# Kernel tuning notes

Hardware: AMD Instinct MI355X
Metric: run time of the kernel (lower is better)

## Reference

```python
import jax, jax.numpy as jnp
import numpy as np

B, T, DIM = 1, 4096, 768
H, D = 6, 128  # num_heads, head_dim
ATTN_SCALE = 0.12
EPS = 1.1920929e-07  # torch fp32 rms_norm default eps


def _rms_norm(x):
    # F.rms_norm over last dim, no learned weight
    return x * jax.lax.rsqrt(jnp.mean(jnp.square(x), axis=-1, keepdims=True) + EPS)


def _rotary_tables(seq_len, head_dim):
    # angular_freq: (1/1024)**linspace(0,1,D//4) concat zeros(D//4) -> length D//2
    af = (1.0 / 1024.0) ** jnp.linspace(0.0, 1.0, head_dim // 4, dtype=jnp.float32)
    af = jnp.concatenate([af, jnp.zeros(head_dim // 4, dtype=jnp.float32)])
    t = jnp.arange(seq_len, dtype=jnp.float32)
    theta = t[:, None] * af[None, :]  # [T, D//2]
    return jnp.cos(theta), jnp.sin(theta)


def _apply_rotary(x_bthd, cos, sin):
    # x: [B,T,H,D]; rotate pairs (x1, x2) = halves of last dim
    x1, x2 = jnp.split(x_bthd.astype(jnp.float32), 2, axis=-1)
    c = cos[None, :, None, :]
    s = sin[None, :, None, :]
    y1 = x1 * c + x2 * s
    y2 = -x1 * s + x2 * c
    return jnp.concatenate([y1, y2], axis=-1).astype(x_bthd.dtype)


def setup_inputs() -> dict:
    key = jax.random.key(0)
    k1, k2, k3, k4, k5 = jax.random.split(key, 5)
    std = 0.5 * DIM ** (-0.5)
    bound = (3.0 ** 0.5) * std
    x = jax.random.normal(k1, (B, T, DIM), dtype=jnp.float32)
    ve = jax.random.normal(k2, (B, T, DIM), dtype=jnp.float32)
    qkv_w = jax.random.uniform(k3, (3, H * D, DIM), dtype=jnp.float32, minval=-bound, maxval=bound)
    lambdas = jnp.array([0.5, 0.5], dtype=jnp.float32)
    # original zero-inits c_proj; use small random weights for a nontrivial output
    c_proj_w = jax.random.uniform(k5, (DIM, H * D), dtype=jnp.float32, minval=-bound, maxval=bound)
    return {"x": x, "ve": ve, "qkv_w": qkv_w, "lambdas": lambdas, "c_proj_w": c_proj_w}


def reference(x, ve, qkv_w, lambdas, c_proj_w):
    Bx, Tx = x.shape[0], x.shape[1]
    # fused QKV: linear with weight [3*hdim, dim] -> [B,T,3*H,D]
    qkv = jnp.einsum('btd,ehd->bteh', x, qkv_w.reshape(3 * H, D, DIM).reshape(3 * H * D, DIM).reshape(3 * H, D, DIM))
    # simpler: flatten weight and reshape output
    w_flat = qkv_w.reshape(3 * H * D, DIM)
    qkv = (x @ w_flat.T).reshape(Bx, Tx, 3 * H, D)
    q, k, v = jnp.split(qkv, 3, axis=2)  # each [B,T,H,D]
    q, k = _rms_norm(q), _rms_norm(k)
    cos, sin = _rotary_tables(Tx, D)
    q, k = _apply_rotary(q, cos, sin), _apply_rotary(k, cos, sin)
    v = lambdas[0] * v + lambdas[1] * ve.reshape(Bx, Tx, H, D)
    # causal attention with non-standard scale
    scores = jnp.einsum('bthd,bshd->bhts', q, k) * ATTN_SCALE  # [B,H,T,T]
    causal = jnp.tril(jnp.ones((Tx, Tx), dtype=bool))
    scores = jnp.where(causal[None, None], scores, -jnp.inf)
    probs = jax.nn.softmax(scores, axis=-1)
    y = jnp.einsum('bhts,bshd->bthd', probs, v).reshape(Bx, Tx, H * D)
    return y @ c_proj_w.T
```

## Files before the change

kernel.cpp:

```cpp
#include <hip/hip_runtime.h>
#include <hip/hip_bf16.h>

using bf16 = __hip_bfloat16;
typedef __attribute__((ext_vector_type(8))) __bf16 bf16x8;
typedef __attribute__((ext_vector_type(4))) float f32x4;

static constexpr int T = 4096, DIM = 768, H = 6, D = 128, N3 = 2304;
static constexpr int PPH = 280;
static constexpr float kEps = 1.1920929e-07f;
static constexpr float kC1 = 0.12f * 1.44269504f;
static constexpr float kTHR = 66.6f;

__device__ __forceinline__ void gll16(const bf16* g, bf16* l) {
  __builtin_amdgcn_global_load_lds((const __attribute__((address_space(1))) void*)g,
                                   (__attribute__((address_space(3))) void*)l, 16, 0, 0);
}

__device__ __forceinline__ int pre_qt(int qt) {
  const int k = qt >> 3, rr = qt & 7;
  return qt + 4 * k * (k - 1) + rr * k;
}

__global__ __launch_bounds__(256) void prep(const float* __restrict__ x,
                                            const float* __restrict__ qkv_w,
                                            const float* __restrict__ cproj,
                                            bf16* __restrict__ xb, bf16* __restrict__ wb,
                                            bf16* __restrict__ cb, float2* __restrict__ tab) {
  const int NBX = T * DIM / 2048, NBW = N3 * DIM / 2048, NBC = DIM * DIM / 2048;
  int b = blockIdx.x;
  const int tid = threadIdx.x;
  if (b < NBX + NBW + NBC) {
    const float* in;
    bf16* out;
    if (b < NBX) { in = x; out = xb; }
    else if (b < NBX + NBW) { in = qkv_w; out = wb; b -= NBX; }
    else { in = cproj; out = cb; b -= NBX + NBW; }
    const int i = (b * 256 + tid) * 8;
    const float4 a = *(const float4*)(in + i);
    const float4 c = *(const float4*)(in + i + 4);
    bf16 t[8] = {(bf16)a.x, (bf16)a.y, (bf16)a.z, (bf16)a.w,
                 (bf16)c.x, (bf16)c.y, (bf16)c.z, (bf16)c.w};
    *(int4*)(out + i) = *(const int4*)t;
  } else {
    b -= NBX + NBW + NBC;
    const int i = b * 256 + tid;
    const int t = i >> 5, j = i & 31;
    const float af = exp2f(-10.f * (float)j * (1.f / 31.f));
    float s, c;
    sincosf((float)t * af, &s, &c);
    tab[i] = make_float2(c, s);
  }
}

template <typename CT>
__global__ __launch_bounds__(256) void gemm_bt(const bf16* __restrict__ A,
                                               const bf16* __restrict__ B,
                                               CT* __restrict__ C,
                                               int M, int N, int K) {
  __shared__ bf16 lA[128][64];
  __shared__ bf16 lB[128][64];
  const int tid = threadIdx.x, lane = tid & 63, wid = tid >> 6;
  const int brow = blockIdx.y * 128, bcol = blockIdx.x * 128;
  const int wm = (wid >> 1) * 64, wn = (wid & 1) * 64;
  const int r = lane & 15, g = lane >> 4;
  f32x4 acc[4][4] = {};
  const int srow = wid * 32 + (lane >> 3);
  const int scol = (lane & 7) * 8;
  const bf16* gA = A + (long)(brow + srow) * K + scol;
  const bf16* gB = B + (long)(bcol + srow) * K + scol;
  for (int k0 = 0; k0 < K; k0 += 64) {
    __syncthreads();
#pragma unroll
    for (int i = 0; i < 4; ++i) {
      gll16(gA + (long)i * 8 * K + k0, &lA[wid * 32 + i * 8][0]);
      gll16(gB + (long)i * 8 * K + k0, &lB[wid * 32 + i * 8][0]);
    }
    __syncthreads();
#pragma unroll
    for (int kk = 0; kk < 2; ++kk) {
      bf16x8 af[4], bfr[4];
#pragma unroll
      for (int m = 0; m < 4; ++m)
        af[m] = *(const bf16x8*)&lA[wm + m * 16 + r][kk * 32 + g * 8];
#pragma unroll
      for (int n = 0; n < 4; ++n)
        bfr[n] = *(const bf16x8*)&lB[wn + n * 16 + r][kk * 32 + g * 8];
#pragma unroll
      for (int m = 0; m < 4; ++m)
#pragma unroll
        for (int n = 0; n < 4; ++n)
          acc[m][n] = __builtin_amdgcn_mfma_f32_16x16x32_bf16(af[m], bfr[n], acc[m][n], 0, 0, 0);
    }
  }
  const int crow = brow + wm + g * 4;
  const int ccol = bcol + wn + r;
#pragma unroll
  for (int m = 0; m < 4; ++m)
#pragma unroll
    for (int n = 0; n < 4; ++n)
#pragma unroll
      for (int q = 0; q < 4; ++q)
        C[(long)(crow + m * 16 + q) * N + ccol + n * 16] = (CT)acc[m][n][q];
}

__global__ __launch_bounds__(256) void qkv_post(const bf16* __restrict__ qkv,
                                                const float2* __restrict__ tab,
                                                bf16* __restrict__ qb,
                                                bf16* __restrict__ kb) {
  const int idx = blockIdx.x * 4 + (threadIdx.x >> 6);
  const int lane = threadIdx.x & 63;
  const int t = idx / H, h = idx % H;
  const bf16* row = qkv + (long)t * N3 + h * D;
  float q1 = __bfloat162float(row[lane]);
  float q2 = __bfloat162float(row[lane + 64]);
  float k1 = __bfloat162float(row[768 + lane]);
  float k2 = __bfloat162float(row[768 + lane + 64]);
  float qs = q1 * q1 + q2 * q2, ks = k1 * k1 + k2 * k2;
#pragma unroll
  for (int off = 32; off; off >>= 1) {
    qs += __shfl_xor(qs, off);
    ks += __shfl_xor(ks, off);
  }
  const float qsc = rsqrtf(qs * (1.f / 128.f) + kEps);
  const float ksc = rsqrtf(ks * (1.f / 128.f) + kEps);
  q1 *= qsc; q2 *= qsc; k1 *= ksc; k2 *= ksc;
  float c = 1.f, s = 0.f;
  if (lane < 32) {
    const float2 cs = tab[t * 32 + lane];
    c = cs.x; s = cs.y;
  }
  const float nq1 = q1 * c + q2 * s, nq2 = q2 * c - q1 * s;
  const float nk1 = k1 * c + k2 * s, nk2 = k2 * c - k1 * s;
  bf16* qo = qb + ((long)h * T + t) * D;
  bf16* ko = kb + ((long)h * T + t) * D;
  qo[lane] = (bf16)nq1; qo[lane + 64] = (bf16)nq2;
  ko[lane] = (bf16)nk1; ko[lane + 64] = (bf16)nk2;
}

__global__ __launch_bounds__(256) void v_trans(const bf16* __restrict__ qkv,
                                               const float* __restrict__ ve,
                                               const float* __restrict__ lam,
                                               bf16* __restrict__ vt) {
  __shared__ bf16 tile[64][129];
  const int t0 = blockIdx.x * 64, h = blockIdx.y;
  const int tid = threadIdx.x;
  const float l0 = lam[0], l1 = lam[1];
  const int row = tid >> 2;
  const int seg = (tid & 3) * 32;
  const bf16* src = qkv + (long)(t0 + row) * N3 + 1536 + h * D + seg;
  const float* vs = ve + (long)(t0 + row) * DIM + h * D + seg;
#pragma unroll
  for (int j = 0; j < 32; j += 8) {
    bf16x8 a = *(const bf16x8*)(src + j);
    const float4 e0 = *(const float4*)(vs + j);
    const float4 e1 = *(const float4*)(vs + j + 4);
    const float ef[8] = {e0.x, e0.y, e0.z, e0.w, e1.x, e1.y, e1.z, e1.w};
#pragma unroll
    for (int u = 0; u < 8; ++u)
      tile[row][seg + j + u] = (bf16)(l0 * (float)a[u] + l1 * ef[u]);
  }
  __syncthreads();
  const int d = tid >> 1, half = tid & 1;
  bf16 outr[32];
#pragma unroll
  for (int j = 0; j < 32; ++j) outr[j] = tile[half * 32 + j][d];
  bf16* dst = vt + ((long)h * D + d) * T + t0 + half * 32;
#pragma unroll
  for (int c = 0; c < 4; ++c)
    *(int4*)(dst + c * 8) = *(const int4*)&outr[c * 8];
}

__global__ __launch_bounds__(512, 4) void attn(const bf16* __restrict__ qb,
                                               const bf16* __restrict__ kb,
                                               const bf16* __restrict__ vt,
                                               bf16* __restrict__ po,
                                               float* __restrict__ pm,
                                               float* __restrict__ ps,
                                               bf16* __restrict__ yb) {
  __shared__ bf16 Kl[64][128];
  __shared__ bf16 Vl[128][64];
  __shared__ bf16 Pl[8][16][64];
  const int bid = blockIdx.x;
  const int h = bid % H;
  const int fi = bid / H;
  int s = 31, ci = 0, acc0 = 0;
  for (int ss = 31; ss >= 0; --ss) {
    const int n = (ss >> 2) + 1;
    if (fi < acc0 + n) { s = ss; ci = fi - acc0; break; }
    acc0 += n;
  }
  const int tid = threadIdx.x, lane = tid & 63, w = tid >> 6;
  const int r = lane & 15, g = lane >> 4;
  const int qt = 2 * s + (w >> 2);
  const int wrow = (w & 3) * 16;
  const int ts = ci * 8;
  const int te = min(ts + 8, 2 * s + 2);

  bf16x8 qf[4];
#pragma unroll
  for (int kk = 0; kk < 4; ++kk)
    qf[kk] = *(const bf16x8*)(qb + ((long)h * T + qt * 64 + wrow + r) * D + kk * 32 + g * 8);
  f32x4 o[8] = {};
  float m[4], sl[4];
#pragma unroll
  for (int q = 0; q < 4; ++q) { m[q] = -1e30f; sl[q] = 0.f; }

  auto STAGE = [&](int t) {
    const int kv0 = t * 64;
#pragma unroll
    for (int i = 0; i < 2; ++i) {
      const int seg = w * 2 + i;
      {
        const int lr = seg * 4 + (lane >> 4);
        const int cs = (lane & 15) ^ (lr & 7);
        gll16(kb + ((long)h * T + kv0 + lr) * D + cs * 8,
              (bf16*)&Kl[0][0] + seg * 512);
      }
      {
        const int lr = seg * 8 + (lane >> 3);
        const int cs = (lane & 7) ^ (lr & 7);
        gll16(vt + ((long)h * D + lr) * T + kv0 + cs * 8,
              (bf16*)&Vl[0][0] + seg * 512);
      }
    }
  };

  STAGE(ts);
  __syncthreads();
  for (int tt = ts; tt < te; ++tt) {
    const bool act = (tt <= qt);
    if (act) {
      const bf16* Kb = (const bf16*)&Kl[0][0];
      const bf16* Vb = (const bf16*)&Vl[0][0];
      bf16* Pb = &Pl[w][0][0];
      f32x4 st4[4];
      __builtin_amdgcn_s_setprio(1);
#pragma unroll
      for (int stt = 0; stt < 4; ++stt) {
        f32x4 a = {};
        const int lrk = stt * 16 + r;
#pragma unroll
        for (int kk = 0; kk < 4; ++kk) {
          const bf16x8 kf = *(const bf16x8*)(Kb + lrk * 128 + (((kk * 4 + g) ^ (lrk & 7)) * 8));
          a = __builtin_amdgcn_mfma_f32_16x16x32_bf16(qf[kk], kf, a, 0, 0, 0);
        }
        st4[stt] = a;
      }
      __builtin_amdgcn_s_setprio(0);
      if (tt == qt) {
        const int qgl = qt * 64 + wrow + 4 * g;
#pragma unroll
        for (int stt = 0; stt < 4; ++stt)
#pragma unroll
          for (int q = 0; q < 4; ++q)
            if (tt * 64 + stt * 16 + r > qgl + q) st4[stt][q] = -1e30f;
      }
      float mx[4];
#pragma unroll
      for (int q = 0; q < 4; ++q)
        mx[q] = fmaxf(fmaxf(st4[0][q], st4[1][q]), fmaxf(st4[2][q], st4[3][q]));
      const float dd = fmaxf(fmaxf(mx[0] - m[0], mx[1] - m[1]),
                             fmaxf(mx[2] - m[2], mx[3] - m[3]));
      if (__any(dd > kTHR)) {
#pragma unroll
        for (int off = 1; off < 16; off <<= 1)
#pragma unroll
          for (int q = 0; q < 4; ++q) mx[q] = fmaxf(mx[q], __shfl_xor(mx[q], off));
#pragma unroll
        for (int q = 0; q < 4; ++q) {
          const float nm = fmaxf(m[q], mx[q]);
          const float al = exp2f((m[q] - nm) * kC1);
          m[q] = nm;
          sl[q] *= al;
#pragma unroll
          for (int nn = 0; nn < 8; ++nn) o[nn][q] *= al;
        }
      }
#pragma unroll
      for (int stt = 0; stt < 4; ++stt)
#pragma unroll
        for (int q = 0; q < 4; ++q)
          st4[stt][q] = exp2f((st4[stt][q] - m[q]) * kC1);
#pragma unroll
      for (int q = 0; q < 4; ++q)
        sl[q] += (st4[0][q] + st4[1][q]) + (st4[2][q] + st4[3][q]);
#pragma unroll
      for (int stt = 0; stt < 4; ++stt)
#pragma unroll
        for (int q = 0; q < 4; ++q) {
          const int rw = 4 * g + q;
          Pb[rw * 64 + ((stt * 16 + r) ^ ((rw & 7) << 3))] = (bf16)st4[stt][q];
        }
      bf16x8 pf[2];
#pragma unroll
      for (int kk = 0; kk < 2; ++kk)
        pf[kk] = *(const bf16x8*)(Pb + r * 64 + (((kk * 4 + g) ^ (r & 7)) * 8));
      __builtin_amdgcn_s_setprio(1);
#pragma unroll
      for (int nn = 0; nn < 8; ++nn) {
        const int d = nn * 16 + r;
#pragma unroll
        for (int kk = 0; kk < 2; ++kk) {
          const bf16x8 vf = *(const bf16x8*)(Vb + d * 64 + (((kk * 4 + g) ^ (d & 7)) * 8));
          o[nn] = __builtin_amdgcn_mfma_f32_16x16x32_bf16(pf[kk], vf, o[nn], 0, 0, 0);
        }
      }
      __builtin_amdgcn_s_setprio(0);
    }
    if (tt + 1 < te) {
      __syncthreads();
      STAGE(tt + 1);
      __syncthreads();
    }
  }
#pragma unroll
  for (int off = 1; off < 16; off <<= 1)
#pragma unroll
    for (int q = 0; q < 4; ++q) sl[q] += __shfl_xor(sl[q], off);
  const int row0 = wrow + 4 * g;
  if (s < 4) {
#pragma unroll
    for (int nn = 0; nn < 8; ++nn)
#pragma unroll
      for (int q = 0; q < 4; ++q)
        yb[(long)(qt * 64 + row0 + q) * DIM + h * D + nn * 16 + r] = (bf16)(o[nn][q] / sl[q]);
  } else {
    const long part = (long)h * PPH + (pre_qt(qt) - 8) + ci;
    bf16* pob = po + part * 8192;
#pragma unroll
    for (int nn = 0; nn < 8; ++nn)
#pragma unroll
      for (int q = 0; q < 4; ++q)
        pob[(row0 + q) * 128 + nn * 16 + r] = (bf16)o[nn][q];
    if (r == 0) {
#pragma unroll
      for (int q = 0; q < 4; ++q) {
        pm[part * 64 + row0 + q] = m[q];
        ps[part * 64 + row0 + q] = sl[q];
      }
    }
  }
}

__global__ __launch_bounds__(256) void attn_reduce(const bf16* __restrict__ po,
                                                   const float* __restrict__ pm,
                                                   const float* __restrict__ ps,
                                                   bf16* __restrict__ yb) {
  const int qt = 8 + blockIdx.x, h = blockIdx.y;
  const int tid = threadIdx.x;
  const int row = tid >> 2, seg = (tid & 3) * 32;
  const int nch = (qt >> 3) + 1;
  const long base = (long)h * PPH + pre_qt(qt) - 8;
  float mm = -1e30f;
  for (int ci = 0; ci < nch; ++ci) mm = fmaxf(mm, pm[(base + ci) * 64 + row]);
  float den = 0.f;
  for (int ci = 0; ci < nch; ++ci)
    den += ps[(base + ci) * 64 + row] * exp2f((pm[(base + ci) * 64 + row] - mm) * kC1);
  const float inv = 1.f / den;
  float acc[32] = {};
  for (int ci = 0; ci < nch; ++ci) {
    const float wq = exp2f((pm[(base + ci) * 64 + row] - mm) * kC1) * inv;
    const bf16* src = po + (base + ci) * 8192 + row * 128 + seg;
#pragma unroll
    for (int j = 0; j < 32; j += 8) {
      const bf16x8 v = *(const bf16x8*)(src + j);
#pragma unroll
      for (int u = 0; u < 8; ++u) acc[j + u] += wq * (float)v[u];
    }
  }
  bf16 outv[32];
#pragma unroll
  for (int j = 0; j < 32; ++j) outv[j] = (bf16)acc[j];
  bf16* dst = yb + (long)(qt * 64 + row) * DIM + h * D + seg;
#pragma unroll
  for (int cc = 0; cc < 4; ++cc)
    *(int4*)(dst + cc * 8) = *(const int4*)&outv[cc * 8];
}

extern "C" void kernel_launch(void* const* d_in, const int* in_sizes, int n_in,
                              void* d_out, int out_size, void* d_ws, size_t ws_size,
                              hipStream_t stream) {
  const float* x     = (const float*)d_in[0];
  const float* ve    = (const float*)d_in[1];
  const float* qkv_w = (const float*)d_in[2];
  const float* lam   = (const float*)d_in[3];
  const float* cproj = (const float*)d_in[4];
  float* out = (float*)d_out;

  bf16* qkv = (bf16*)d_ws;
  bf16* xb  = qkv + (long)T * N3;
  bf16* wb  = xb + (long)T * DIM;
  bf16* cb  = wb + (long)N3 * DIM;
  bf16* qb  = cb + (long)DIM * DIM;
  bf16* kb  = qb + (long)H * T * D;
  bf16* vt  = kb + (long)H * T * D;
  bf16* yb  = vt + (long)H * T * D;
  float2* tab = (float2*)(yb + (long)T * DIM);
  bf16* po  = (bf16*)d_ws;
  float* pm = (float*)(po + (long)PPH * H * 8192);
  float* ps = pm + (long)PPH * H * 64;

  const int NBX = T * DIM / 2048, NBW = N3 * DIM / 2048, NBC = DIM * DIM / 2048;
  prep<<<dim3(NBX + NBW + NBC + T * 32 / 256), 256, 0, stream>>>(x, qkv_w, cproj, xb, wb, cb, tab);

  gemm_bt<bf16><<<dim3(N3 / 128, T / 128), 256, 0, stream>>>(xb, wb, qkv, T, N3, DIM);
  qkv_post<<<dim3(T * H / 4), 256, 0, stream>>>(qkv, tab, qb, kb);
  v_trans<<<dim3(T / 64, H), 256, 0, stream>>>(qkv, ve, lam, vt);
  attn<<<dim3(144 * H), 512, 0, stream>>>(qb, kb, vt, po, pm, ps, yb);
  attn_reduce<<<dim3(56, H), 256, 0, stream>>>(po, pm, ps, yb);
  gemm_bt<float><<<dim3(DIM / 128, T / 128), 256, 0, stream>>>(yb, cb, out, T, DIM, DIM);
}
```

Baseline: 154.2 us.

## Double-buffer K/V tiles in attention and fold softmax scale into Q

```diff
diff --git a/kernel.cpp b/kernel.cpp
--- a/kernel.cpp
+++ b/kernel.cpp
@@ -9,7 +9,7 @@
 static constexpr int PPH = 280;
 static constexpr float kEps = 1.1920929e-07f;
 static constexpr float kC1 = 0.12f * 1.44269504f;
-static constexpr float kTHR = 66.6f;
+static constexpr float kTHR = 11.54f;
 
 __device__ __forceinline__ void gll16(const bf16* g, bf16* l) {
   __builtin_amdgcn_global_load_lds((const __attribute__((address_space(1))) void*)g,
@@ -121,7 +121,7 @@
     qs += __shfl_xor(qs, off);
     ks += __shfl_xor(ks, off);
   }
-  const float qsc = rsqrtf(qs * (1.f / 128.f) + kEps);
+  const float qsc = rsqrtf(qs * (1.f / 128.f) + kEps) * kC1;
   const float ksc = rsqrtf(ks * (1.f / 128.f) + kEps);
   q1 *= qsc; q2 *= qsc; k1 *= ksc; k2 *= ksc;
   float c = 1.f, s = 0.f;
@@ -170,15 +170,15 @@
     *(int4*)(dst + c * 8) = *(const int4*)&outr[c * 8];
 }
 
-__global__ __launch_bounds__(512, 4) void attn(const bf16* __restrict__ qb,
+__global__ __launch_bounds__(512, 2) void attn(const bf16* __restrict__ qb,
                                                const bf16* __restrict__ kb,
                                                const bf16* __restrict__ vt,
                                                bf16* __restrict__ po,
                                                float* __restrict__ pm,
                                                float* __restrict__ ps,
                                                bf16* __restrict__ yb) {
-  __shared__ bf16 Kl[64][128];
-  __shared__ bf16 Vl[128][64];
+  __shared__ bf16 Kl[2][64][128];
+  __shared__ bf16 Vl[2][128][64];
   __shared__ bf16 Pl[8][16][64];
   const int bid = blockIdx.x;
   const int h = bid % H;
@@ -205,7 +205,7 @@
 #pragma unroll
   for (int q = 0; q < 4; ++q) { m[q] = -1e30f; sl[q] = 0.f; }
 
-  auto STAGE = [&](int t) {
+  auto STAGE = [&](int buf, int t) {
     const int kv0 = t * 64;
 #pragma unroll
     for (int i = 0; i < 2; ++i) {
@@ -214,24 +214,26 @@
         const int lr = seg * 4 + (lane >> 4);
         const int cs = (lane & 15) ^ (lr & 7);
         gll16(kb + ((long)h * T + kv0 + lr) * D + cs * 8,
-              (bf16*)&Kl[0][0] + seg * 512);
+              (bf16*)&Kl[buf][0][0] + seg * 512);
       }
       {
         const int lr = seg * 8 + (lane >> 3);
         const int cs = (lane & 7) ^ (lr & 7);
         gll16(vt + ((long)h * D + lr) * T + kv0 + cs * 8,
-              (bf16*)&Vl[0][0] + seg * 512);
+              (bf16*)&Vl[buf][0][0] + seg * 512);
       }
     }
   };
 
-  STAGE(ts);
+  STAGE(0, ts);
   __syncthreads();
+  int cur = 0;
   for (int tt = ts; tt < te; ++tt) {
+    if (tt + 1 < te) STAGE(cur ^ 1, tt + 1);
     const bool act = (tt <= qt);
     if (act) {
-      const bf16* Kb = (const bf16*)&Kl[0][0];
-      const bf16* Vb = (const bf16*)&Vl[0][0];
+      const bf16* Kb = (const bf16*)&Kl[cur][0][0];
+      const bf16* Vb = (const bf16*)&Vl[cur][0][0];
       bf16* Pb = &Pl[w][0][0];
       f32x4 st4[4];
       __builtin_amdgcn_s_setprio(1);
@@ -269,7 +271,7 @@
 #pragma unroll
         for (int q = 0; q < 4; ++q) {
           const float nm = fmaxf(m[q], mx[q]);
-          const float al = exp2f((m[q] - nm) * kC1);
+          const float al = exp2f(m[q] - nm);
           m[q] = nm;
           sl[q] *= al;
 #pragma unroll
@@ -280,7 +282,7 @@
       for (int stt = 0; stt < 4; ++stt)
 #pragma unroll
         for (int q = 0; q < 4; ++q)
-          st4[stt][q] = exp2f((st4[stt][q] - m[q]) * kC1);
+          st4[stt][q] = exp2f(st4[stt][q] - m[q]);
 #pragma unroll
       for (int q = 0; q < 4; ++q)
         sl[q] += (st4[0][q] + st4[1][q]) + (st4[2][q] + st4[3][q]);
@@ -307,11 +309,8 @@
       }
       __builtin_amdgcn_s_setprio(0);
     }
-    if (tt + 1 < te) {
-      __syncthreads();
-      STAGE(tt + 1);
-      __syncthreads();
-    }
+    __syncthreads();
+    cur ^= 1;
   }
 #pragma unroll
   for (int off = 1; off < 16; off <<= 1)
@@ -355,11 +354,11 @@
   for (int ci = 0; ci < nch; ++ci) mm = fmaxf(mm, pm[(base + ci) * 64 + row]);
   float den = 0.f;
   for (int ci = 0; ci < nch; ++ci)
-    den += ps[(base + ci) * 64 + row] * exp2f((pm[(base + ci) * 64 + row] - mm) * kC1);
+    den += ps[(base + ci) * 64 + row] * exp2f(pm[(base + ci) * 64 + row] - mm);
   const float inv = 1.f / den;
   float acc[32] = {};
   for (int ci = 0; ci < nch; ++ci) {
-    const float wq = exp2f((pm[(base + ci) * 64 + row] - mm) * kC1) * inv;
+    const float wq = exp2f(pm[(base + ci) * 64 + row] - mm) * inv;
     const bf16* src = po + (base + ci) * 8192 + row * 128 + seg;
 #pragma unroll
     for (int j = 0; j < 32; j += 8) {
```

Result: slower. 174.8 us (+13.4%).
